# Performance work log

Measured on AMD Instinct MI355X. Metric: run time of the kernel, lower is better.

Reference implementation:

```python
import jax, jax.numpy as jnp
import numpy as np

B, S, K, N = 4, 2048, 4096, 4096

def setup_inputs() -> dict:
    key = jax.random.key(0)
    k1, k2, k3, k4 = jax.random.split(key, 4)
    # int8 quantized activations and weight (stored as int8, matmul accumulates int32)
    a = jax.random.randint(k1, (B, S, K), -128, 128, dtype=jnp.int32).astype(jnp.int8)
    w = jax.random.randint(k3, (K, N), -128, 128, dtype=jnp.int32).astype(jnp.int8)
    # dequant scales: per-token for activations, per-output-channel for weight
    a_s = (jax.random.uniform(k2, (B, S, 1), dtype=jnp.float32) + 0.5) * 0.01
    w_s = (jax.random.uniform(k4, (1, N), dtype=jnp.float32) + 0.5) * 0.01
    return {"a": a, "a_s": a_s, "w": w, "w_s": w_s}

def reference(a, a_s, w, w_s):
    # torch._int_mm loop with padding), fused with dequant epilogue.
    acc = jnp.einsum('bsk,kn->bsn', a, w, preferred_element_type=jnp.int32)
    # dequant: float32 accum * input_scale * weight_scale, cast to model dtype (fp16)
    out = (acc.astype(jnp.float32) * a_s * w_s).astype(jnp.float16)
    return out
```

## Files before the change

### kernel.cpp

```cpp
#include <hip/hip_runtime.h>
#include <cstdint>
#include <cstddef>


#define M_DIM 8192
#define N_DIM 4096
#define K_DIM 4096

#define PREP_A_BLOCKS ((M_DIM / 32) * (K_DIM / 128))
#define PREP_W_BLOCKS ((N_DIM / 64) * (K_DIM / 64))

typedef int v4i  __attribute__((ext_vector_type(4)));
typedef int v16i __attribute__((ext_vector_type(16)));

__device__ __forceinline__ uint32_t pack4(int x, int y, int z, int w)
{
    return (uint32_t)(x & 0xff) | ((uint32_t)(y & 0xff) << 8) |
           ((uint32_t)(z & 0xff) << 16) | ((uint32_t)(w & 0xff) << 24);
}

__global__ void __launch_bounds__(256) prepare_kernel(
    const int* __restrict__ a, const int* __restrict__ w,
    uint8_t* __restrict__ a_f, uint8_t* __restrict__ w_f)
{
    __shared__ int lds[64][65];
    const int t = threadIdx.x;

    if (blockIdx.x < PREP_A_BLOCKS) {
        uint32_t* l32 = (uint32_t*)&lds[0][0];
        const int bm = blockIdx.x >> 5;
        const int bk = blockIdx.x & 31;
        const int m0 = bm * 32;
        const int k0 = bk * 128;
#pragma unroll
        for (int i = 0; i < 4; ++i) {
            const int f = i * 256 + t;
            const int r = f >> 5;
            const int c = (f << 2) & 127;
            int4 x = *(const int4*)(a + (size_t)(m0 + r) * K_DIM + k0 + c);
            uint32_t u = pack4(x.x, x.y, x.z, x.w);
            const int region = c >> 5;
            const int chunk  = r + (((c >> 4) & 1) << 5);
            const int wd     = region * 256 + chunk * 4 + ((c & 15) >> 2);
            l32[wd ^ ((region & 3) << 3)] = u;
        }
        __syncthreads();
        uint4 o = ((const uint4*)l32)[t ^ (((t >> 6) & 3) << 1)];
        *(uint4*)(a_f + ((size_t)bm * 128 + bk * 4) * 1024 + t * 16) = o;
        return;
    }

    const int tile = blockIdx.x - PREP_A_BLOCKS;
    const int n0 = (tile & 63) * 64;
    const int k0 = (tile >> 6) * 64;

#pragma unroll
    for (int i = 0; i < 4; ++i) {
        int v   = t + 256 * i;
        int row = v >> 4;
        int cq  = v & 15;
        int4 x = *(const int4*)(w + (size_t)(k0 + row) * N_DIM + n0 + cq * 4);
        lds[row][cq * 4 + 0] = x.x;
        lds[row][cq * 4 + 1] = x.y;
        lds[row][cq * 4 + 2] = x.z;
        lds[row][cq * 4 + 3] = x.w;
    }
    __syncthreads();

    const int chunk  = t & 63;
    const int r_out  = t >> 6;
    const int nb     = r_out >> 1;
    const int kk     = r_out & 1;
    const int ncol   = nb * 32 + (chunk & 31);
    const int parity = chunk >> 5;
    const int rbase  = kk * 32 + parity * 16;
    uint32_t o[4];
#pragma unroll
    for (int q = 0; q < 4; ++q)
        o[q] = pack4(lds[rbase + q * 4 + 0][ncol],
                     lds[rbase + q * 4 + 1][ncol],
                     lds[rbase + q * 4 + 2][ncol],
                     lds[rbase + q * 4 + 3][ncol]);
    *(uint4*)(w_f + (((size_t)(n0 >> 5) + nb) * 128 + (k0 >> 5) + kk) * 1024
                  + chunk * 16) = make_uint4(o[0], o[1], o[2], o[3]);
}

__device__ __forceinline__ void async_copy16(const void* gptr, void* lptr)
{
    __builtin_amdgcn_global_load_lds(
        (const __attribute__((address_space(1))) uint32_t*)gptr,
        (__attribute__((address_space(3))) uint32_t*)lptr,
        16, 0, 0);
}

#define WAIT_VMCNT0() asm volatile("s_waitcnt vmcnt(0)" ::: "memory")
#define SCHED_FENCE() __builtin_amdgcn_sched_barrier(0)

__global__ void __launch_bounds__(512, 2) int8_gemm_kernel(
    const uint8_t* __restrict__ Af,
    const uint8_t* __restrict__ Wf,
    const float*   __restrict__ a_s,
    const float*   __restrict__ w_s,
    float*         __restrict__ out)
{
    __shared__ __align__(16) uint8_t sA[2][4][8][1024];
    __shared__ __align__(16) uint8_t sB[2][4][8][1024];

    const int tid   = threadIdx.x;
    const int wave  = tid >> 6;
    const int lane  = tid & 63;
    const int waveM = wave >> 2;
    const int waveN = wave & 3;

    const int bid = blockIdx.x;
    const int xc  = bid & 7;
    const int j   = bid >> 3;
    const int bm  = (xc & 3) * 8 + (j & 7);
    const int bn  = (xc >> 2) * 8 + (j >> 3);
    const int m0  = bm * 256;
    const int n0  = bn * 256;

    v16i acc[4][2];
#pragma unroll
    for (int i = 0; i < 4; ++i)
#pragma unroll
        for (int jj = 0; jj < 2; ++jj)
#pragma unroll
            for (int r = 0; r < 16; ++r)
                acc[i][jj][r] = 0;

    const uint8_t* aBase = Af + (((size_t)(m0 >> 5) + wave) * 128) * 1024 + lane * 16;
    const uint8_t* bBase = Wf + (((size_t)(n0 >> 5) + wave) * 128) * 1024 + lane * 16;

    auto stage_pair = [&](int buf, int kt, int s) {
        async_copy16(aBase + (size_t)(kt * 4 + s) * 1024, &sA[buf][s][wave][0]);
        async_copy16(bBase + (size_t)(kt * 4 + s) * 1024, &sB[buf][s][wave][0]);
    };

    auto ds_read6 = [&](v4i (&af)[4], v4i (&bf)[2], int buf, int s) {
#pragma unroll
        for (int mt = 0; mt < 4; ++mt)
            af[mt] = *(const v4i*)(&sA[buf][s][waveM * 4 + mt][lane * 16]);
#pragma unroll
        for (int nt = 0; nt < 2; ++nt)
            bf[nt] = *(const v4i*)(&sB[buf][s][waveN * 2 + nt][lane * 16]);
    };

    auto mfma8 = [&](v4i (&af)[4], v4i (&bf)[2]) {
        __builtin_amdgcn_s_setprio(1);
#pragma unroll
        for (int mt = 0; mt < 4; ++mt)
#pragma unroll
            for (int nt = 0; nt < 2; ++nt)
                acc[mt][nt] = __builtin_amdgcn_mfma_i32_32x32x32_i8(
                    af[mt], bf[nt], acc[mt][nt], 0, 0, 0);
        __builtin_amdgcn_s_setprio(0);
    };

    const int NT = K_DIM / 128;

    v4i afA[4], bfA[2], afB[4], bfB[2];

#pragma unroll
    for (int s = 0; s < 4; ++s)
        stage_pair(0, 0, s);
    WAIT_VMCNT0();
    SCHED_FENCE();
    __builtin_amdgcn_s_barrier();
    ds_read6(afA, bfA, 0, 0);

    for (int kt = 0; kt < NT - 1; ++kt) {
        const int b = kt & 1;
        stage_pair(b ^ 1, kt + 1, 0);
        ds_read6(afB, bfB, b, 1);
        SCHED_FENCE();
        mfma8(afA, bfA);
        SCHED_FENCE();
        stage_pair(b ^ 1, kt + 1, 1);
        ds_read6(afA, bfA, b, 2);
        SCHED_FENCE();
        mfma8(afB, bfB);
        SCHED_FENCE();
        stage_pair(b ^ 1, kt + 1, 2);
        ds_read6(afB, bfB, b, 3);
        SCHED_FENCE();
        mfma8(afA, bfA);
        SCHED_FENCE();
        stage_pair(b ^ 1, kt + 1, 3);
        SCHED_FENCE();
        mfma8(afB, bfB);
        SCHED_FENCE();
        WAIT_VMCNT0();
        SCHED_FENCE();
        __builtin_amdgcn_s_barrier();
        ds_read6(afA, bfA, b ^ 1, 0);
    }

    {
        const int b = (NT - 1) & 1;
        ds_read6(afB, bfB, b, 1);
        SCHED_FENCE();
        mfma8(afA, bfA);
        SCHED_FENCE();
        ds_read6(afA, bfA, b, 2);
        SCHED_FENCE();
        mfma8(afB, bfB);
        SCHED_FENCE();
        ds_read6(afB, bfB, b, 3);
        SCHED_FENCE();
        mfma8(afA, bfA);
        SCHED_FENCE();
        mfma8(afB, bfB);
    }

    const int col   = lane & 31;
    const int rbase = (lane >> 5) * 4;

#pragma unroll
    for (int mt = 0; mt < 4; ++mt) {
        const int mrow0 = m0 + waveM * 128 + mt * 32 + rbase;
        float asv[16];
#pragma unroll
        for (int reg = 0; reg < 16; ++reg)
            asv[reg] = a_s[mrow0 + (reg & 3) + 8 * (reg >> 2)];
#pragma unroll
        for (int nt = 0; nt < 2; ++nt) {
            const int n = n0 + waveN * 64 + nt * 32 + col;
            const float wsv = w_s[n];
#pragma unroll
            for (int reg = 0; reg < 16; ++reg) {
                const int row = mrow0 + (reg & 3) + 8 * (reg >> 2);
                float v = (float)acc[mt][nt][reg] * asv[reg] * wsv;
                v = (float)(_Float16)v;
                out[(size_t)row * N_DIM + n] = v;
            }
        }
    }
}

extern "C" void kernel_launch(void* const* d_in, const int* in_sizes, int n_in,
                              void* d_out, int out_size, void* d_ws, size_t ws_size,
                              hipStream_t stream)
{
    const int*   a   = (const int*)  d_in[0];
    const float* a_s = (const float*)d_in[1];
    const int*   w   = (const int*)  d_in[2];
    const float* w_s = (const float*)d_in[3];
    float*       out = (float*)d_out;

    uint8_t* w_f = (uint8_t*)d_ws;
    uint8_t* a_f = (uint8_t*)d_ws + (size_t)N_DIM * K_DIM;

    prepare_kernel<<<PREP_A_BLOCKS + PREP_W_BLOCKS, 256, 0, stream>>>(
        a, w, a_f, w_f);

    int8_gemm_kernel<<<(M_DIM / 256) * (N_DIM / 256), 512, 0, stream>>>(
        a_f, w_f, a_s, w_s, out);
}
```

Before: 409.1 us.

## Replace full vmcnt drain with fine-grained per-substage waits and barriers

Replaces the single vmcnt(0) wait and barrier at the end of each K tile with partial vmcnt(4) waits and an extra pair of workgroup barriers around every MFMA group. This lets each 1 KB LDS sub-stage be consumed as soon as its async copy lands, so global loads stay in flight across the tile boundary. In exchange it adds eight s_barriers per tile, which can stall waves and interfere with the ping-pong scheduling of the two co-resident blocks.

```diff
diff --git a/kernel.cpp b/kernel.cpp
--- a/kernel.cpp
+++ b/kernel.cpp
@@ -93,7 +93,7 @@
         16, 0, 0);
 }
 
-#define WAIT_VMCNT0() asm volatile("s_waitcnt vmcnt(0)" ::: "memory")
+#define WAIT_VMCNT(n) asm volatile("s_waitcnt vmcnt(" #n ")" ::: "memory")
 #define SCHED_FENCE() __builtin_amdgcn_sched_barrier(0)
 
 __global__ void __launch_bounds__(512, 2) int8_gemm_kernel(
@@ -159,58 +159,85 @@
 
     const int NT = K_DIM / 128;
 
-    v4i afA[4], bfA[2], afB[4], bfB[2];
+    v4i afP[4], bfP[2], afN[4], bfN[2];
 
 #pragma unroll
     for (int s = 0; s < 4; ++s)
         stage_pair(0, 0, s);
-    WAIT_VMCNT0();
+    WAIT_VMCNT(4);
     SCHED_FENCE();
     __builtin_amdgcn_s_barrier();
-    ds_read6(afA, bfA, 0, 0);
+    ds_read6(afP, bfP, 0, 0);
 
     for (int kt = 0; kt < NT - 1; ++kt) {
         const int b = kt & 1;
         stage_pair(b ^ 1, kt + 1, 0);
-        ds_read6(afB, bfB, b, 1);
-        SCHED_FENCE();
-        mfma8(afA, bfA);
+        ds_read6(afN, bfN, b, 1);
+        SCHED_FENCE();
+        __builtin_amdgcn_s_barrier();
+        SCHED_FENCE();
+        mfma8(afP, bfP);
+        WAIT_VMCNT(4);
+        SCHED_FENCE();
+        __builtin_amdgcn_s_barrier();
         SCHED_FENCE();
         stage_pair(b ^ 1, kt + 1, 1);
-        ds_read6(afA, bfA, b, 2);
-        SCHED_FENCE();
-        mfma8(afB, bfB);
+        ds_read6(afP, bfP, b, 2);
+        SCHED_FENCE();
+        __builtin_amdgcn_s_barrier();
+        SCHED_FENCE();
+        mfma8(afN, bfN);
+        WAIT_VMCNT(4);
+        SCHED_FENCE();
+        __builtin_amdgcn_s_barrier();
         SCHED_FENCE();
         stage_pair(b ^ 1, kt + 1, 2);
-        ds_read6(afB, bfB, b, 3);
-        SCHED_FENCE();
-        mfma8(afA, bfA);
+        ds_read6(afN, bfN, b, 3);
+        SCHED_FENCE();
+        __builtin_amdgcn_s_barrier();
+        SCHED_FENCE();
+        mfma8(afP, bfP);
+        WAIT_VMCNT(4);
+        SCHED_FENCE();
+        __builtin_amdgcn_s_barrier();
         SCHED_FENCE();
         stage_pair(b ^ 1, kt + 1, 3);
-        SCHED_FENCE();
-        mfma8(afB, bfB);
-        SCHED_FENCE();
-        WAIT_VMCNT0();
-        SCHED_FENCE();
-        __builtin_amdgcn_s_barrier();
-        ds_read6(afA, bfA, b ^ 1, 0);
+        ds_read6(afP, bfP, b ^ 1, 0);
+        SCHED_FENCE();
+        __builtin_amdgcn_s_barrier();
+        SCHED_FENCE();
+        mfma8(afN, bfN);
+        WAIT_VMCNT(4);
+        SCHED_FENCE();
+        __builtin_amdgcn_s_barrier();
+        SCHED_FENCE();
     }
 
     {
         const int b = (NT - 1) & 1;
-        ds_read6(afB, bfB, b, 1);
-        SCHED_FENCE();
-        mfma8(afA, bfA);
-        SCHED_FENCE();
-        ds_read6(afA, bfA, b, 2);
-        SCHED_FENCE();
-        mfma8(afB, bfB);
-        SCHED_FENCE();
-        ds_read6(afB, bfB, b, 3);
-        SCHED_FENCE();
-        mfma8(afA, bfA);
-        SCHED_FENCE();
-        mfma8(afB, bfB);
+        ds_read6(afN, bfN, b, 1);
+        SCHED_FENCE();
+        __builtin_amdgcn_s_barrier();
+        SCHED_FENCE();
+        mfma8(afP, bfP);
+        WAIT_VMCNT(2);
+        SCHED_FENCE();
+        __builtin_amdgcn_s_barrier();
+        SCHED_FENCE();
+        ds_read6(afP, bfP, b, 2);
+        SCHED_FENCE();
+        __builtin_amdgcn_s_barrier();
+        SCHED_FENCE();
+        mfma8(afN, bfN);
+        WAIT_VMCNT(0);
+        SCHED_FENCE();
+        __builtin_amdgcn_s_barrier();
+        SCHED_FENCE();
+        ds_read6(afN, bfN, b, 3);
+        SCHED_FENCE();
+        mfma8(afP, bfP);
+        SCHED_FENCE();
+        mfma8(afN, bfN);
     }
 
     const int col   = lane & 31;
```

Result: slower. 426.9 us (+4.4%).
